# Kernel tuning notes

Measured on AMD Instinct MI355X. Metric: run time of the kernel, lower is better.

## Reference

```python
import jax, jax.numpy as jnp
import numpy as np

WINDOW_SIZE = 11
SIGMA = 1.5

def _gaussian_window():
    x = np.arange(WINDOW_SIZE, dtype=np.float64) - WINDOW_SIZE // 2
    g = np.exp(-(x ** 2) / (2.0 * SIGMA ** 2))
    g = (g / g.sum()).astype(np.float32)
    w2 = np.outer(g, g)  # [11, 11]
    return jnp.asarray(w2)


def setup_inputs() -> dict:
    key = jax.random.key(0)
    k1, k2 = jax.random.split(key)
    B, C, H, W = 32, 3, 512, 512
    img1 = jax.random.uniform(k1, (B, C, H, W), dtype=jnp.float32)
    img2 = jax.random.uniform(k2, (B, C, H, W), dtype=jnp.float32)
    return {"img1": img1, "img2": img2}


def reference(img1, img2):
    # peak = 1.0, size_average = True
    c1 = jnp.float32(0.01 ** 2)
    c2 = jnp.float32(0.03 ** 2)
    C = img1.shape[1]
    w2 = _gaussian_window()

    # One fused depthwise conv over the 5 statistic planes (same math as 5
    # separate grouped convs in the original).
    stacked = jnp.concatenate(
        [img1, img2, img1 * img1, img2 * img2, img1 * img2], axis=1
    )  # [B, 5C, H, W]
    kernel = jnp.tile(w2[None, None], (5 * C, 1, 1, 1))  # [5C, 1, 11, 11]
    out = jax.lax.conv_general_dilated(
        stacked, kernel,
        window_strides=(1, 1), padding='VALID',
        feature_group_count=5 * C,
        dimension_numbers=('NCHW', 'OIHW', 'NCHW'),
    )  # [B, 5C, H-10, W-10]

    mu1 = out[:, 0 * C:1 * C]
    mu2 = out[:, 1 * C:2 * C]
    mu1_sq = mu1 * mu1
    mu2_sq = mu2 * mu2
    mu1_mu2 = mu1 * mu2
    sigma1_sq = out[:, 2 * C:3 * C] - mu1_sq
    sigma2_sq = out[:, 3 * C:4 * C] - mu2_sq
    sigma12 = out[:, 4 * C:5 * C] - mu1_mu2

    ssim_map = ((2 * mu1_mu2 + c1) * (2 * sigma12 + c2)) / (
        (mu1_sq + mu2_sq + c1) * (sigma1_sq + sigma2_sq + c2)
    )
    return jnp.mean(ssim_map)
```

## Files before the change

kernel.cpp:

```cpp
#include <hip/hip_runtime.h>


namespace {
constexpr int IMG_H = 512;
constexpr int IMG_W = 512;
constexpr int NIMG  = 96;
constexpr int OUT_H = 502;
constexpr int OUT_W = 502;
constexpr int RPB   = 64;
constexpr int QR    = 4;
constexpr int BUFW  = 544;
constexpr double TOTAL = 24192384.0;

constexpr double U0 = 0.0038659201;
constexpr double U1 = 0.0285655007;
constexpr double U2 = 0.1353352832366127;
constexpr double U3 = 0.4111122898;
constexpr double U4 = 0.8007374026;
constexpr double S  = 1.0 + 2.0 * (U0 + U1 + U2 + U3 + U4);
}

__device__ __forceinline__ float2 f2fma(float w, float2 a, float2 c) {
    return make_float2(fmaf(w, a.x, c.x), fmaf(w, a.y, c.y));
}

__global__ __launch_bounds__(256, 3) void ssim_main(const float* __restrict__ img1,
                                                    const float* __restrict__ img2,
                                                    double* __restrict__ acc)
{
    __shared__ __align__(16) float vrow[QR][5][BUFW];
    __shared__ float red[4];

    const float g[11] = {
        (float)(U0/S), (float)(U1/S), (float)(U2/S), (float)(U3/S), (float)(U4/S),
        (float)(1.0/S),
        (float)(U4/S), (float)(U3/S), (float)(U2/S), (float)(U1/S), (float)(U0/S)
    };
    constexpr float C1 = 1e-4f;
    constexpr float C2 = 9e-4f;

    const int t   = threadIdx.x;
    const int z   = blockIdx.y;
    const int oy0 = blockIdx.x * RPB;
    const int row_end = min(oy0 + RPB, OUT_H);

    const float* p1 = img1 + (size_t)z * (IMG_H * IMG_W);
    const float* p2 = img2 + (size_t)z * (IMG_H * IMG_W);

    const int c4w  = t >> 1;
    const int woff = ((c4w ^ ((c4w >> 3) & 7)) << 2) + ((t & 1) << 1);

    const int hq = t >> 6;
    const int hl = t & 63;
    const int cb = hl << 3;
    int roff[5];
    #pragma unroll
    for (int k = 0; k < 5; ++k) {
        int c4 = (cb >> 2) + k;
        roff[k] = (c4 ^ ((c4 >> 3) & 7)) << 2;
    }

    float local = 0.f;

    for (int r0 = oy0; r0 < row_end; r0 += QR) {
        float2 xr[QR + 10], yr[QR + 10];
        #pragma unroll
        for (int j = 0; j < QR + 10; ++j) {
            int row = r0 + j;
            row = row < IMG_H ? row : IMG_H - 1;
            const float2* a = (const float2*)(p1 + (size_t)row * IMG_W);
            const float2* b = (const float2*)(p2 + (size_t)row * IMG_W);
            xr[j] = a[t];
            yr[j] = b[t];
        }
        float2 vm1[QR], vm2[QR], v11[QR], v22[QR], v12[QR];
        #pragma unroll
        for (int q = 0; q < QR; ++q) {
            vm1[q] = make_float2(0.f, 0.f);
            vm2[q] = make_float2(0.f, 0.f);
            v11[q] = make_float2(0.f, 0.f);
            v22[q] = make_float2(0.f, 0.f);
            v12[q] = make_float2(0.f, 0.f);
        }
        #pragma unroll
        for (int j = 0; j < QR + 10; ++j) {
            float2 x = xr[j], y = yr[j];
            float2 xx = make_float2(x.x * x.x, x.y * x.y);
            float2 yy = make_float2(y.x * y.x, y.y * y.y);
            float2 xy = make_float2(x.x * y.x, x.y * y.y);
            #pragma unroll
            for (int q = 0; q < QR; ++q) {
                int k = j - q;
                if (k >= 0 && k < 11) {
                    float w = g[k];
                    vm1[q] = f2fma(w, x,  vm1[q]);
                    vm2[q] = f2fma(w, y,  vm2[q]);
                    v11[q] = f2fma(w, xx, v11[q]);
                    v22[q] = f2fma(w, yy, v22[q]);
                    v12[q] = f2fma(w, xy, v12[q]);
                }
            }
        }
        __syncthreads();
        #pragma unroll
        for (int q = 0; q < QR; ++q) {
            *(float2*)&vrow[q][0][woff] = vm1[q];
            *(float2*)&vrow[q][1][woff] = vm2[q];
            *(float2*)&vrow[q][2][woff] = v11[q];
            *(float2*)&vrow[q][3][woff] = v22[q];
            *(float2*)&vrow[q][4][woff] = v12[q];
        }
        __syncthreads();

        const int rr = r0 + hq;
        if (rr < row_end && cb < OUT_W) {
            float aa[5][8];
            #pragma unroll
            for (int ch = 0; ch < 5; ++ch) {
                const float* bc = &vrow[hq][ch][0];
                float f[20];
                #pragma unroll
                for (int k = 0; k < 5; ++k) {
                    float4 v = *(const float4*)(bc + roff[k]);
                    f[4*k+0] = v.x; f[4*k+1] = v.y; f[4*k+2] = v.z; f[4*k+3] = v.w;
                }
                #pragma unroll
                for (int j = 0; j < 8; ++j) {
                    float s = 0.f;
                    #pragma unroll
                    for (int k = 0; k < 11; ++k) s = fmaf(g[k], f[j + k], s);
                    aa[ch][j] = s;
                }
            }
            #pragma unroll
            for (int j = 0; j < 8; ++j) {
                if (cb + j < OUT_W) {
                    float mu1 = aa[0][j], mu2 = aa[1][j];
                    float e11 = aa[2][j], e22 = aa[3][j], e12 = aa[4][j];
                    float mu11 = mu1 * mu1;
                    float mu22 = mu2 * mu2;
                    float mu12 = mu1 * mu2;
                    float s1  = e11 - mu11;
                    float s2  = e22 - mu22;
                    float s12 = e12 - mu12;
                    float num = fmaf(2.f, mu12, C1) * fmaf(2.f, s12, C2);
                    float den = (mu11 + mu22 + C1) * (s1 + s2 + C2);
                    local += num / den;
                }
            }
        }
    }

    #pragma unroll
    for (int off = 32; off > 0; off >>= 1) local += __shfl_down(local, off, 64);
    if ((t & 63) == 0) red[t >> 6] = local;
    __syncthreads();
    if (t == 0) {
        double s = (double)red[0] + (double)red[1] + (double)red[2] + (double)red[3];
        atomicAdd(acc, s);
    }
}

__global__ void ssim_fin(const double* __restrict__ acc, float* __restrict__ out)
{
    out[0] = (float)(acc[0] / TOTAL);
}

extern "C" void kernel_launch(void* const* d_in, const int* in_sizes, int n_in,
                              void* d_out, int out_size, void* d_ws, size_t ws_size,
                              hipStream_t stream)
{
    (void)in_sizes; (void)n_in; (void)out_size; (void)ws_size;
    const float* img1 = (const float*)d_in[0];
    const float* img2 = (const float*)d_in[1];
    double* acc = (double*)d_ws;

    hipMemsetAsync(d_ws, 0, sizeof(double), stream);
    dim3 grid((OUT_H + RPB - 1) / RPB, NIMG);
    hipLaunchKernelGGL(ssim_main, grid, dim3(256), 0, stream, img1, img2, acc);
    hipLaunchKernelGGL(ssim_fin, dim3(1), dim3(1), 0, stream, acc, (float*)d_out);
}
```

Before: 271.2 us.

## Rewrite SSIM as single-wavefront strips with sliding register window and shuffles

Replaces the 256-thread block with LDS staging by 64-thread blocks. Each block handles a 100-column strip and 63-row band. Vertical filtering uses a sliding 12-row register window that computes two output rows per step, and horizontal filtering uses cross-lane shuffles instead of shared memory. The change also swaps the divide for a refined hardware reciprocal and replaces the double atomic with per-block partials reduced by a final kernel. Strip halos are loaded redundantly through overlapping columns, and lanes past the strip edge do wasted work.

```diff
diff --git a/kernel.cpp b/kernel.cpp
--- a/kernel.cpp
+++ b/kernel.cpp
@@ -2,14 +2,13 @@
 
 
 namespace {
-constexpr int IMG_H = 512;
-constexpr int IMG_W = 512;
-constexpr int NIMG  = 96;
-constexpr int OUT_H = 502;
-constexpr int OUT_W = 502;
-constexpr int RPB   = 64;
-constexpr int QR    = 4;
-constexpr int BUFW  = 544;
+constexpr int IMG_H = 512, IMG_W = 512;
+constexpr int OUT_H = 502, OUT_W = 502;
+constexpr int NIMG   = 96;
+constexpr int NSTRIP = 5;
+constexpr int NBAND  = 8;
+constexpr int RB     = 63;
+constexpr int NTASK  = NIMG * NSTRIP * NBAND;
 constexpr double TOTAL = 24192384.0;
 
 constexpr double U0 = 0.0038659201;
@@ -17,153 +16,173 @@
 constexpr double U2 = 0.1353352832366127;
 constexpr double U3 = 0.4111122898;
 constexpr double U4 = 0.8007374026;
-constexpr double S  = 1.0 + 2.0 * (U0 + U1 + U2 + U3 + U4);
+constexpr double SS = 1.0 + 2.0 * (U0 + U1 + U2 + U3 + U4);
 }
 
-__device__ __forceinline__ float2 f2fma(float w, float2 a, float2 c) {
-    return make_float2(fmaf(w, a.x, c.x), fmaf(w, a.y, c.y));
-}
+#define G_DEF const float g[11] = { \
+    (float)(U0/SS), (float)(U1/SS), (float)(U2/SS), (float)(U3/SS), (float)(U4/SS), \
+    (float)(1.0/SS), \
+    (float)(U4/SS), (float)(U3/SS), (float)(U2/SS), (float)(U1/SS), (float)(U0/SS) }
 
-__global__ __launch_bounds__(256, 3) void ssim_main(const float* __restrict__ img1,
-                                                    const float* __restrict__ img2,
-                                                    double* __restrict__ acc)
+__device__ __forceinline__ void hssim(const float2 v[5], const float g[11], int lane,
+                                      bool va, bool vb, float& acc0, float& acc1)
 {
-    __shared__ __align__(16) float vrow[QR][5][BUFW];
-    __shared__ float red[4];
-
-    const float g[11] = {
-        (float)(U0/S), (float)(U1/S), (float)(U2/S), (float)(U3/S), (float)(U4/S),
-        (float)(1.0/S),
-        (float)(U4/S), (float)(U3/S), (float)(U2/S), (float)(U1/S), (float)(U0/S)
-    };
-    constexpr float C1 = 1e-4f;
-    constexpr float C2 = 9e-4f;
-
-    const int t   = threadIdx.x;
-    const int z   = blockIdx.y;
-    const int oy0 = blockIdx.x * RPB;
-    const int row_end = min(oy0 + RPB, OUT_H);
-
-    const float* p1 = img1 + (size_t)z * (IMG_H * IMG_W);
-    const float* p2 = img2 + (size_t)z * (IMG_H * IMG_W);
-
-    const int c4w  = t >> 1;
-    const int woff = ((c4w ^ ((c4w >> 3) & 7)) << 2) + ((t & 1) << 1);
-
-    const int hq = t >> 6;
-    const int hl = t & 63;
-    const int cb = hl << 3;
-    int roff[5];
+    float h0[5], h1[5];
     #pragma unroll
-    for (int k = 0; k < 5; ++k) {
-        int c4 = (cb >> 2) + k;
-        roff[k] = (c4 ^ ((c4 >> 3) & 7)) << 2;
+    for (int i = 0; i < 5; ++i) {
+        float a[12];
+        a[0] = v[i].x; a[1] = v[i].y;
+        #pragma unroll
+        for (int d = 1; d <= 5; ++d) {
+            a[2*d]     = __shfl(v[i].x, lane + d, 64);
+            a[2*d + 1] = __shfl(v[i].y, lane + d, 64);
+        }
+        float s0 = 0.f, s1 = 0.f;
+        #pragma unroll
+        for (int k = 0; k < 11; ++k) {
+            s0 = fmaf(g[k], a[k],     s0);
+            s1 = fmaf(g[k], a[k + 1], s1);
+        }
+        h0[i] = s0; h1[i] = s1;
     }
-
-    float local = 0.f;
-
-    for (int r0 = oy0; r0 < row_end; r0 += QR) {
-        float2 xr[QR + 10], yr[QR + 10];
-        #pragma unroll
-        for (int j = 0; j < QR + 10; ++j) {
-            int row = r0 + j;
-            row = row < IMG_H ? row : IMG_H - 1;
-            const float2* a = (const float2*)(p1 + (size_t)row * IMG_W);
-            const float2* b = (const float2*)(p2 + (size_t)row * IMG_W);
-            xr[j] = a[t];
-            yr[j] = b[t];
-        }
-        float2 vm1[QR], vm2[QR], v11[QR], v22[QR], v12[QR];
-        #pragma unroll
-        for (int q = 0; q < QR; ++q) {
-            vm1[q] = make_float2(0.f, 0.f);
-            vm2[q] = make_float2(0.f, 0.f);
-            v11[q] = make_float2(0.f, 0.f);
-            v22[q] = make_float2(0.f, 0.f);
-            v12[q] = make_float2(0.f, 0.f);
-        }
-        #pragma unroll
-        for (int j = 0; j < QR + 10; ++j) {
-            float2 x = xr[j], y = yr[j];
-            float2 xx = make_float2(x.x * x.x, x.y * x.y);
-            float2 yy = make_float2(y.x * y.x, y.y * y.y);
-            float2 xy = make_float2(x.x * y.x, x.y * y.y);
-            #pragma unroll
-            for (int q = 0; q < QR; ++q) {
-                int k = j - q;
-                if (k >= 0 && k < 11) {
-                    float w = g[k];
-                    vm1[q] = f2fma(w, x,  vm1[q]);
-                    vm2[q] = f2fma(w, y,  vm2[q]);
-                    v11[q] = f2fma(w, xx, v11[q]);
-                    v22[q] = f2fma(w, yy, v22[q]);
-                    v12[q] = f2fma(w, xy, v12[q]);
-                }
-            }
-        }
-        __syncthreads();
-        #pragma unroll
-        for (int q = 0; q < QR; ++q) {
-            *(float2*)&vrow[q][0][woff] = vm1[q];
-            *(float2*)&vrow[q][1][woff] = vm2[q];
-            *(float2*)&vrow[q][2][woff] = v11[q];
-            *(float2*)&vrow[q][3][woff] = v22[q];
-            *(float2*)&vrow[q][4][woff] = v12[q];
-        }
-        __syncthreads();
-
-        const int rr = r0 + hq;
-        if (rr < row_end && cb < OUT_W) {
-            float aa[5][8];
-            #pragma unroll
-            for (int ch = 0; ch < 5; ++ch) {
-                const float* bc = &vrow[hq][ch][0];
-                float f[20];
-                #pragma unroll
-                for (int k = 0; k < 5; ++k) {
-                    float4 v = *(const float4*)(bc + roff[k]);
-                    f[4*k+0] = v.x; f[4*k+1] = v.y; f[4*k+2] = v.z; f[4*k+3] = v.w;
-                }
-                #pragma unroll
-                for (int j = 0; j < 8; ++j) {
-                    float s = 0.f;
-                    #pragma unroll
-                    for (int k = 0; k < 11; ++k) s = fmaf(g[k], f[j + k], s);
-                    aa[ch][j] = s;
-                }
-            }
-            #pragma unroll
-            for (int j = 0; j < 8; ++j) {
-                if (cb + j < OUT_W) {
-                    float mu1 = aa[0][j], mu2 = aa[1][j];
-                    float e11 = aa[2][j], e22 = aa[3][j], e12 = aa[4][j];
-                    float mu11 = mu1 * mu1;
-                    float mu22 = mu2 * mu2;
-                    float mu12 = mu1 * mu2;
-                    float s1  = e11 - mu11;
-                    float s2  = e22 - mu22;
-                    float s12 = e12 - mu12;
-                    float num = fmaf(2.f, mu12, C1) * fmaf(2.f, s12, C2);
-                    float den = (mu11 + mu22 + C1) * (s1 + s2 + C2);
-                    local += num / den;
-                }
-            }
-        }
+    constexpr float C1 = 1e-4f, C2 = 9e-4f;
+    {
+        float mu1 = h0[0], mu2 = h0[1];
+        float mu11 = mu1*mu1, mu22 = mu2*mu2, mu12 = mu1*mu2;
+        float s1 = h0[2] - mu11, s2 = h0[3] - mu22, s12 = h0[4] - mu12;
+        float num = fmaf(2.f, mu12, C1) * fmaf(2.f, s12, C2);
+        float den = (mu11 + mu22 + C1) * (s1 + s2 + C2);
+        float rc = __builtin_amdgcn_rcpf(den);
+        rc = rc * fmaf(-den, rc, 2.f);
+        float val = num * rc;
+        acc0 += va ? val : 0.f;
     }
-
-    #pragma unroll
-    for (int off = 32; off > 0; off >>= 1) local += __shfl_down(local, off, 64);
-    if ((t & 63) == 0) red[t >> 6] = local;
-    __syncthreads();
-    if (t == 0) {
-        double s = (double)red[0] + (double)red[1] + (double)red[2] + (double)red[3];
-        atomicAdd(acc, s);
+    {
+        float mu1 = h1[0], mu2 = h1[1];
+        float mu11 = mu1*mu1, mu22 = mu2*mu2, mu12 = mu1*mu2;
+        float s1 = h1[2] - mu11, s2 = h1[3] - mu22, s12 = h1[4] - mu12;
+        float num = fmaf(2.f, mu12, C1) * fmaf(2.f, s12, C2);
+        float den = (mu11 + mu22 + C1) * (s1 + s2 + C2);
+        float rc = __builtin_amdgcn_rcpf(den);
+        rc = rc * fmaf(-den, rc, 2.f);
+        float val = num * rc;
+        acc1 += vb ? val : 0.f;
     }
 }
 
-__global__ void ssim_fin(const double* __restrict__ acc, float* __restrict__ out)
+__global__ __launch_bounds__(64, 3) void ssim_main(const float* __restrict__ img1,
+                                                   const float* __restrict__ img2,
+                                                   float* __restrict__ partial)
 {
-    out[0] = (float)(acc[0] / TOTAL);
+    G_DEF;
+    const int t    = threadIdx.x;
+    const int task = blockIdx.x;
+    const int z    = task / (NSTRIP * NBAND);
+    const int rem  = task - z * (NSTRIP * NBAND);
+    const int s    = rem / NBAND;
+    const int b    = rem - s * NBAND;
+
+    const int lo = 100 * s;
+    const int hi = (s == NSTRIP - 1) ? OUT_W : lo + 100;
+    const int r0 = RB * b;
+    const int r1 = min(r0 + RB, OUT_H);
+
+    const int  o0 = lo + 2 * t;
+    const bool va = (o0     < hi);
+    const bool vb = (o0 + 1 < hi);
+
+    const int col = min(o0, IMG_W - 2);
+    const float* p1 = img1 + (size_t)z * (IMG_H * IMG_W) + col;
+    const float* p2 = img2 + (size_t)z * (IMG_H * IMG_W) + col;
+
+    float2 wx[12], wy[12];
+    #pragma unroll
+    for (int j = 0; j < 12; ++j) {
+        wx[j] = *(const float2*)(p1 + (size_t)(r0 + j) * IMG_W);
+        wy[j] = *(const float2*)(p2 + (size_t)(r0 + j) * IMG_W);
+    }
+
+    float acc0 = 0.f, acc1 = 0.f;
+
+    int r = r0;
+    for (; r + 1 < r1; r += 2) {
+        const int ra = min(r + 12, IMG_H - 1);
+        const int rb2 = min(r + 13, IMG_H - 1);
+        float2 nx0 = *(const float2*)(p1 + (size_t)ra  * IMG_W);
+        float2 ny0 = *(const float2*)(p2 + (size_t)ra  * IMG_W);
+        float2 nx1 = *(const float2*)(p1 + (size_t)rb2 * IMG_W);
+        float2 ny1 = *(const float2*)(p2 + (size_t)rb2 * IMG_W);
+
+        float2 vA[5], vB[5];
+        #pragma unroll
+        for (int i = 0; i < 5; ++i) { vA[i] = make_float2(0.f, 0.f); vB[i] = make_float2(0.f, 0.f); }
+        #pragma unroll
+        for (int k = 0; k < 12; ++k) {
+            float2 x = wx[k], y = wy[k];
+            float xx0 = x.x*x.x, xx1 = x.y*x.y;
+            float yy0 = y.x*y.x, yy1 = y.y*y.y;
+            float xy0 = x.x*y.x, xy1 = x.y*y.y;
+            if (k < 11) {
+                float gk = g[k];
+                vA[0].x = fmaf(gk, x.x, vA[0].x); vA[0].y = fmaf(gk, x.y, vA[0].y);
+                vA[1].x = fmaf(gk, y.x, vA[1].x); vA[1].y = fmaf(gk, y.y, vA[1].y);
+                vA[2].x = fmaf(gk, xx0, vA[2].x); vA[2].y = fmaf(gk, xx1, vA[2].y);
+                vA[3].x = fmaf(gk, yy0, vA[3].x); vA[3].y = fmaf(gk, yy1, vA[3].y);
+                vA[4].x = fmaf(gk, xy0, vA[4].x); vA[4].y = fmaf(gk, xy1, vA[4].y);
+            }
+            if (k >= 1) {
+                float gk = g[k - 1];
+                vB[0].x = fmaf(gk, x.x, vB[0].x); vB[0].y = fmaf(gk, x.y, vB[0].y);
+                vB[1].x = fmaf(gk, y.x, vB[1].x); vB[1].y = fmaf(gk, y.y, vB[1].y);
+                vB[2].x = fmaf(gk, xx0, vB[2].x); vB[2].y = fmaf(gk, xx1, vB[2].y);
+                vB[3].x = fmaf(gk, yy0, vB[3].x); vB[3].y = fmaf(gk, yy1, vB[3].y);
+                vB[4].x = fmaf(gk, xy0, vB[4].x); vB[4].y = fmaf(gk, xy1, vB[4].y);
+            }
+        }
+
+        hssim(vA, g, t, va, vb, acc0, acc1);
+        hssim(vB, g, t, va, vb, acc0, acc1);
+
+        #pragma unroll
+        for (int k = 0; k < 10; ++k) { wx[k] = wx[k + 2]; wy[k] = wy[k + 2]; }
+        wx[10] = nx0; wy[10] = ny0; wx[11] = nx1; wy[11] = ny1;
+    }
+
+    if (r < r1) {
+        float2 vA[5];
+        #pragma unroll
+        for (int i = 0; i < 5; ++i) vA[i] = make_float2(0.f, 0.f);
+        #pragma unroll
+        for (int k = 0; k < 11; ++k) {
+            float2 x = wx[k], y = wy[k];
+            float gk = g[k];
+            vA[0].x = fmaf(gk, x.x, vA[0].x);       vA[0].y = fmaf(gk, x.y, vA[0].y);
+            vA[1].x = fmaf(gk, y.x, vA[1].x);       vA[1].y = fmaf(gk, y.y, vA[1].y);
+            vA[2].x = fmaf(gk, x.x*x.x, vA[2].x);   vA[2].y = fmaf(gk, x.y*x.y, vA[2].y);
+            vA[3].x = fmaf(gk, y.x*y.x, vA[3].x);   vA[3].y = fmaf(gk, y.y*y.y, vA[3].y);
+            vA[4].x = fmaf(gk, x.x*y.x, vA[4].x);   vA[4].y = fmaf(gk, x.y*y.y, vA[4].y);
+        }
+        hssim(vA, g, t, va, vb, acc0, acc1);
+    }
+
+    float local = acc0 + acc1;
+    #pragma unroll
+    for (int off = 32; off > 0; off >>= 1) local += __shfl_down(local, off, 64);
+    if (t == 0) partial[task] = local;
+}
+
+__global__ void ssim_fin(const float* __restrict__ partial, float* __restrict__ out)
+{
+    __shared__ double sd[256];
+    double sum = 0.0;
+    for (int i = threadIdx.x; i < NTASK; i += 256) sum += (double)partial[i];
+    sd[threadIdx.x] = sum;
+    __syncthreads();
+    for (int w = 128; w > 0; w >>= 1) {
+        if (threadIdx.x < w) sd[threadIdx.x] += sd[threadIdx.x + w];
+        __syncthreads();
+    }
+    if (threadIdx.x == 0) out[0] = (float)(sd[0] / TOTAL);
 }
 
 extern "C" void kernel_launch(void* const* d_in, const int* in_sizes, int n_in,
@@ -173,10 +192,8 @@
     (void)in_sizes; (void)n_in; (void)out_size; (void)ws_size;
     const float* img1 = (const float*)d_in[0];
     const float* img2 = (const float*)d_in[1];
-    double* acc = (double*)d_ws;
+    float* partial = (float*)d_ws;
 
-    hipMemsetAsync(d_ws, 0, sizeof(double), stream);
-    dim3 grid((OUT_H + RPB - 1) / RPB, NIMG);
-    hipLaunchKernelGGL(ssim_main, grid, dim3(256), 0, stream, img1, img2, acc);
-    hipLaunchKernelGGL(ssim_fin, dim3(1), dim3(1), 0, stream, acc, (float*)d_out);
+    hipLaunchKernelGGL(ssim_main, dim3(NTASK), dim3(64), 0, stream, img1, img2, partial);
+    hipLaunchKernelGGL(ssim_fin, dim3(1), dim3(256), 0, stream, partial, (float*)d_out);
 }
```

After: 315.1 us. 1.16x slower.

## Shrink row bands, raise occupancy, use fast reciprocal and per-block partial sums

Applied to the files above, without the earlier changes.

Halves rows per block to 32 across 16 bands and cuts rows per iteration from 4 to 3. This shrinks shared memory and registers so the launch bound can target 5 blocks per SM. The double atomicAdd and memset are replaced by per-block float partials summed by a 256-thread finisher kernel. The divide becomes a hardware reciprocal with one Newton step, and the LDS swizzle is simplified. With QR=3 one of the four wavefronts sits idle in the horizontal pass, and each row iteration now reloads 13 input rows to produce 3 outputs, which adds global traffic.

```diff
diff --git a/kernel.cpp b/kernel.cpp
--- a/kernel.cpp
+++ b/kernel.cpp
@@ -2,14 +2,14 @@
 
 
 namespace {
-constexpr int IMG_H = 512;
-constexpr int IMG_W = 512;
+constexpr int IMG_H = 512, IMG_W = 512;
+constexpr int OUT_H = 502, OUT_W = 502;
 constexpr int NIMG  = 96;
-constexpr int OUT_H = 502;
-constexpr int OUT_W = 502;
-constexpr int RPB   = 64;
-constexpr int QR    = 4;
-constexpr int BUFW  = 544;
+constexpr int RPB   = 32;
+constexpr int NBAND = 16;
+constexpr int QR    = 3;
+constexpr int BUFW  = 528;
+constexpr int NTASK = NBAND * NIMG;
 constexpr double TOTAL = 24192384.0;
 
 constexpr double U0 = 0.0038659201;
@@ -17,27 +17,28 @@
 constexpr double U2 = 0.1353352832366127;
 constexpr double U3 = 0.4111122898;
 constexpr double U4 = 0.8007374026;
-constexpr double S  = 1.0 + 2.0 * (U0 + U1 + U2 + U3 + U4);
+constexpr double SS = 1.0 + 2.0 * (U0 + U1 + U2 + U3 + U4);
 }
+
+__device__ __forceinline__ int sw(int c4) { return c4 ^ ((c4 >> 3) & 1); }
 
 __device__ __forceinline__ float2 f2fma(float w, float2 a, float2 c) {
     return make_float2(fmaf(w, a.x, c.x), fmaf(w, a.y, c.y));
 }
 
-__global__ __launch_bounds__(256, 3) void ssim_main(const float* __restrict__ img1,
+__global__ __launch_bounds__(256, 5) void ssim_main(const float* __restrict__ img1,
                                                     const float* __restrict__ img2,
-                                                    double* __restrict__ acc)
+                                                    float* __restrict__ partial)
 {
     __shared__ __align__(16) float vrow[QR][5][BUFW];
     __shared__ float red[4];
 
     const float g[11] = {
-        (float)(U0/S), (float)(U1/S), (float)(U2/S), (float)(U3/S), (float)(U4/S),
-        (float)(1.0/S),
-        (float)(U4/S), (float)(U3/S), (float)(U2/S), (float)(U1/S), (float)(U0/S)
+        (float)(U0/SS), (float)(U1/SS), (float)(U2/SS), (float)(U3/SS), (float)(U4/SS),
+        (float)(1.0/SS),
+        (float)(U4/SS), (float)(U3/SS), (float)(U2/SS), (float)(U1/SS), (float)(U0/SS)
     };
-    constexpr float C1 = 1e-4f;
-    constexpr float C2 = 9e-4f;
+    constexpr float C1 = 1e-4f, C2 = 9e-4f;
 
     const int t   = threadIdx.x;
     const int z   = blockIdx.y;
@@ -47,18 +48,14 @@
     const float* p1 = img1 + (size_t)z * (IMG_H * IMG_W);
     const float* p2 = img2 + (size_t)z * (IMG_H * IMG_W);
 
-    const int c4w  = t >> 1;
-    const int woff = ((c4w ^ ((c4w >> 3) & 7)) << 2) + ((t & 1) << 1);
+    const int woff = (sw(t >> 1) << 2) + ((t & 1) << 1);
 
     const int hq = t >> 6;
     const int hl = t & 63;
     const int cb = hl << 3;
     int roff[5];
     #pragma unroll
-    for (int k = 0; k < 5; ++k) {
-        int c4 = (cb >> 2) + k;
-        roff[k] = (c4 ^ ((c4 >> 3) & 7)) << 2;
-    }
+    for (int k = 0; k < 5; ++k) roff[k] = sw((cb >> 2) + k) << 2;
 
     float local = 0.f;
 
@@ -68,18 +65,14 @@
         for (int j = 0; j < QR + 10; ++j) {
             int row = r0 + j;
             row = row < IMG_H ? row : IMG_H - 1;
-            const float2* a = (const float2*)(p1 + (size_t)row * IMG_W);
-            const float2* b = (const float2*)(p2 + (size_t)row * IMG_W);
-            xr[j] = a[t];
-            yr[j] = b[t];
+            xr[j] = *(const float2*)(p1 + (size_t)row * IMG_W + 2 * t);
+            yr[j] = *(const float2*)(p2 + (size_t)row * IMG_W + 2 * t);
         }
         float2 vm1[QR], vm2[QR], v11[QR], v22[QR], v12[QR];
         #pragma unroll
         for (int q = 0; q < QR; ++q) {
-            vm1[q] = make_float2(0.f, 0.f);
-            vm2[q] = make_float2(0.f, 0.f);
-            v11[q] = make_float2(0.f, 0.f);
-            v22[q] = make_float2(0.f, 0.f);
+            vm1[q] = make_float2(0.f, 0.f); vm2[q] = make_float2(0.f, 0.f);
+            v11[q] = make_float2(0.f, 0.f); v22[q] = make_float2(0.f, 0.f);
             v12[q] = make_float2(0.f, 0.f);
         }
         #pragma unroll
@@ -113,7 +106,7 @@
         __syncthreads();
 
         const int rr = r0 + hq;
-        if (rr < row_end && cb < OUT_W) {
+        if (hq < QR && rr < row_end && cb < OUT_W) {
             float aa[5][8];
             #pragma unroll
             for (int ch = 0; ch < 5; ++ch) {
@@ -136,16 +129,15 @@
             for (int j = 0; j < 8; ++j) {
                 if (cb + j < OUT_W) {
                     float mu1 = aa[0][j], mu2 = aa[1][j];
-                    float e11 = aa[2][j], e22 = aa[3][j], e12 = aa[4][j];
-                    float mu11 = mu1 * mu1;
-                    float mu22 = mu2 * mu2;
-                    float mu12 = mu1 * mu2;
-                    float s1  = e11 - mu11;
-                    float s2  = e22 - mu22;
-                    float s12 = e12 - mu12;
+                    float mu11 = mu1 * mu1, mu22 = mu2 * mu2, mu12 = mu1 * mu2;
+                    float s1  = aa[2][j] - mu11;
+                    float s2  = aa[3][j] - mu22;
+                    float s12 = aa[4][j] - mu12;
                     float num = fmaf(2.f, mu12, C1) * fmaf(2.f, s12, C2);
                     float den = (mu11 + mu22 + C1) * (s1 + s2 + C2);
-                    local += num / den;
+                    float rc  = __builtin_amdgcn_rcpf(den);
+                    rc = rc * fmaf(-den, rc, 2.f);
+                    local += num * rc;
                 }
             }
         }
@@ -155,15 +147,22 @@
     for (int off = 32; off > 0; off >>= 1) local += __shfl_down(local, off, 64);
     if ((t & 63) == 0) red[t >> 6] = local;
     __syncthreads();
-    if (t == 0) {
-        double s = (double)red[0] + (double)red[1] + (double)red[2] + (double)red[3];
-        atomicAdd(acc, s);
-    }
+    if (t == 0)
+        partial[blockIdx.y * NBAND + blockIdx.x] = red[0] + red[1] + red[2] + red[3];
 }
 
-__global__ void ssim_fin(const double* __restrict__ acc, float* __restrict__ out)
+__global__ void ssim_fin(const float* __restrict__ partial, float* __restrict__ out)
 {
-    out[0] = (float)(acc[0] / TOTAL);
+    __shared__ double sd[256];
+    double sum = 0.0;
+    for (int i = threadIdx.x; i < NTASK; i += 256) sum += (double)partial[i];
+    sd[threadIdx.x] = sum;
+    __syncthreads();
+    for (int w = 128; w > 0; w >>= 1) {
+        if (threadIdx.x < w) sd[threadIdx.x] += sd[threadIdx.x + w];
+        __syncthreads();
+    }
+    if (threadIdx.x == 0) out[0] = (float)(sd[0] / TOTAL);
 }
 
 extern "C" void kernel_launch(void* const* d_in, const int* in_sizes, int n_in,
@@ -173,10 +172,10 @@
     (void)in_sizes; (void)n_in; (void)out_size; (void)ws_size;
     const float* img1 = (const float*)d_in[0];
     const float* img2 = (const float*)d_in[1];
-    double* acc = (double*)d_ws;
+    float* partial = (float*)d_ws;
 
-    hipMemsetAsync(d_ws, 0, sizeof(double), stream);
-    dim3 grid((OUT_H + RPB - 1) / RPB, NIMG);
-    hipLaunchKernelGGL(ssim_main, grid, dim3(256), 0, stream, img1, img2, acc);
-    hipLaunchKernelGGL(ssim_fin, dim3(1), dim3(1), 0, stream, acc, (float*)d_out);
+    hipLaunchKernelGGL(ssim_main, dim3(NBAND, NIMG), dim3(256), 0, stream,
+                       img1, img2, partial);
+    hipLaunchKernelGGL(ssim_fin, dim3(1), dim3(256), 0, stream,
+                       partial, (float*)d_out);
 }
```

Result: slower. 302.9 us (+11.7%).
